# Performance work log

Hardware: AMD Instinct MI355X
Metric: run time of the kernel (lower is better)

The kernel has to match this reference:

```python
import jax, jax.numpy as jnp
import numpy as np

EPS = 1e-8

def setup_inputs() -> dict:
    key = jax.random.key(0)
    k1, k2, k3, k4, k5 = jax.random.split(key, 5)
    B, S, d, H = 4, 1024, 512, 8
    hd = d // H
    x = jax.random.normal(k1, (B, S, d), dtype=jnp.float32)
    V = jax.random.normal(k2, (B, S, H, hd), dtype=jnp.float32)
    # binary biological mask [B, S, S]
    M = (jax.random.uniform(k3, (B, S, S)) > 0.5).astype(jnp.float32)
    in_proj_w = jax.random.normal(k4, (3 * d, d), dtype=jnp.float32) * 0.02
    in_proj_b = jnp.zeros((3 * d,), dtype=jnp.float32)
    out_w = jax.random.normal(k5, (d, d), dtype=jnp.float32) * 0.02
    out_b = jnp.zeros((d,), dtype=jnp.float32)
    return {"x": x, "V": V, "M": M, "in_proj_w": in_proj_w,
            "in_proj_b": in_proj_b, "out_w": out_w, "out_b": out_b}


def reference(x, V, M, in_proj_w, in_proj_b, out_w, out_b):
    B, S, d = x.shape
    H, hd = V.shape[2], V.shape[3]
    # packed QKV projection (torch MHA in_proj); V slice is computed by torch
    # but its result is discarded, so only Q,K slices influence the output.
    qkv = x @ in_proj_w.T + in_proj_b            # [B, S, 3d]
    q = qkv[..., :d].reshape(B, S, H, hd).transpose(0, 2, 1, 3)        # [B,H,S,hd]
    k = qkv[..., d:2 * d].reshape(B, S, H, hd).transpose(0, 2, 1, 3)   # [B,H,S,hd]
    scores = jnp.einsum("bhqd,bhkd->bhqk", q, k) / jnp.sqrt(jnp.float32(hd))
    A = jax.nn.softmax(scores, axis=-1)           # [B,H,S,S] per-head attn weights
    # biological mask + L1 renormalization (post-hoc, as in original)
    A_sparse = A * M[:, None, :, :]
    norm = jnp.sum(jnp.abs(A_sparse), axis=-1, keepdims=True) + EPS
    A_bar = A_sparse / norm
    # custom V: [B,S,H,hd] -> [B,H,S,hd]
    Vp = V.transpose(0, 2, 1, 3)
    out = jnp.einsum("bhqk,bhkd->bhqd", A_bar, Vp)  # [B,H,S,hd]
    out = out.transpose(0, 2, 1, 3).reshape(B, S, d)
    return out @ out_w.T + out_b
```

## Files before the change

kernel.cpp:

```cpp
#include <hip/hip_runtime.h>
#include <hip/hip_bf16.h>

#define BB 4
#define SS 1024
#define DD 512
#define HH 8
#define HD 64

typedef __attribute__((ext_vector_type(8))) short bf16x8;
typedef __attribute__((ext_vector_type(4))) float f32x4;

static __device__ __forceinline__ unsigned short f2b(float f) {
  union { float f; unsigned int u; } c; c.f = f;
  return (unsigned short)((c.u + 0x7fffu + ((c.u >> 16) & 1u)) >> 16);
}

__global__ __launch_bounds__(256) void prep(
    const float* __restrict__ x, const float* __restrict__ W1,
    const float* __restrict__ Wo, const float* __restrict__ Mmask,
    const float* __restrict__ V, unsigned short* __restrict__ xb,
    unsigned short* __restrict__ W1b, unsigned short* __restrict__ Wob,
    unsigned char* __restrict__ Mpack, unsigned short* __restrict__ Vt) {
  __shared__ float Ls[64][65];
  const int bid = blockIdx.x;
  const int tid = threadIdx.x;

  if (bid < 1408) {
    const float* src; unsigned short* dst; size_t off;
    if (bid < 1024) { src = x;  dst = xb;  off = ((size_t)bid * 256 + tid) * 8; }
    else if (bid < 1280) { src = W1; dst = W1b; off = ((size_t)(bid - 1024) * 256 + tid) * 8; }
    else { src = Wo; dst = Wob; off = ((size_t)(bid - 1280) * 256 + tid) * 8; }
    const float4 a = *(const float4*)(src + off);
    const float4 b = *(const float4*)(src + off + 4);
    union { unsigned short s[8]; uint4 v; } o;
    o.s[0] = f2b(a.x); o.s[1] = f2b(a.y); o.s[2] = f2b(a.z); o.s[3] = f2b(a.w);
    o.s[4] = f2b(b.x); o.s[5] = f2b(b.y); o.s[6] = f2b(b.z); o.s[7] = f2b(b.w);
    *(uint4*)(dst + off) = o.v;
  } else if (bid < 3456) {
    const size_t g = (size_t)(bid - 1408) * 256 + tid;
    const float4 a = *(const float4*)(Mmask + g * 8);
    const float4 b = *(const float4*)(Mmask + g * 8 + 4);
    unsigned v = 0;
    v |= (a.x > 0.5f) ? 1u : 0u;   v |= (a.y > 0.5f) ? 2u : 0u;
    v |= (a.z > 0.5f) ? 4u : 0u;   v |= (a.w > 0.5f) ? 8u : 0u;
    v |= (b.x > 0.5f) ? 16u : 0u;  v |= (b.y > 0.5f) ? 32u : 0u;
    v |= (b.z > 0.5f) ? 64u : 0u;  v |= (b.w > 0.5f) ? 128u : 0u;
    Mpack[g] = (unsigned char)v;
  } else {
    const int id = bid - 3456;
    const int s0 = (id & 15) * 64, h = (id >> 4) & 7, b = id >> 7;
    {
      const int r = tid >> 2, cs = (tid & 3) * 16;
      const float* src = V + ((size_t)((b * SS + s0 + r) * HH) + h) * HD + cs;
#pragma unroll
      for (int j = 0; j < 4; j++) {
        const float4 v = *(const float4*)(src + j * 4);
        Ls[r][cs + j * 4 + 0] = v.x; Ls[r][cs + j * 4 + 1] = v.y;
        Ls[r][cs + j * 4 + 2] = v.z; Ls[r][cs + j * 4 + 3] = v.w;
      }
    }
    __syncthreads();
    {
      const int d = tid >> 2, ss = (tid & 3) * 16;
      union { unsigned short s[16]; uint4 v[2]; } o;
#pragma unroll
      for (int j = 0; j < 16; j++) o.s[j] = f2b(Ls[ss + j][d]);
      unsigned short* dst =
          Vt + ((size_t)((b * HH + h) * HD + d)) * SS + s0 + ss;
      *(uint4*)dst = o.v[0];
      *(uint4*)(dst + 8) = o.v[1];
    }
  }
}

__global__ __launch_bounds__(256) void gemm_qk(
    const unsigned short* __restrict__ xb, const unsigned short* __restrict__ W1b,
    const float* __restrict__ bias, unsigned short* __restrict__ qkb) {
  __shared__ unsigned short As[128][40];
  __shared__ unsigned short Bs[64][40];
  const int tid = threadIdx.x;
  const int lane = tid & 63, wave = tid >> 6;
  const int l16 = lane & 15, quad = lane >> 4;
  const int row0 = blockIdx.y * 128, col0 = blockIdx.x * 64;

  f32x4 acc[2][4];
#pragma unroll
  for (int i = 0; i < 2; i++)
#pragma unroll
    for (int j = 0; j < 4; j++) acc[i][j] = (f32x4){0.f, 0.f, 0.f, 0.f};

  const int ra = tid >> 1, csa = (tid & 1) * 16;
  const int rb = tid >> 2, csb = (tid & 3) * 8;
  const unsigned short* ap = xb + (size_t)(row0 + ra) * DD + csa;
  const unsigned short* bp = W1b + (size_t)(col0 + rb) * DD + csb;

  uint4 pa0 = *(const uint4*)ap, pa1 = *(const uint4*)(ap + 8);
  uint4 pb = *(const uint4*)bp;

  for (int k0 = 0; k0 < DD; k0 += 32) {
    __syncthreads();
    *(uint4*)&As[ra][csa] = pa0;
    *(uint4*)&As[ra][csa + 8] = pa1;
    *(uint4*)&Bs[rb][csb] = pb;
    __syncthreads();
    if (k0 + 32 < DD) {
      pa0 = *(const uint4*)(ap + k0 + 32);
      pa1 = *(const uint4*)(ap + k0 + 40);
      pb = *(const uint4*)(bp + k0 + 32);
    }

    const bf16x8 a0 = *(const bf16x8*)&As[wave * 32 + l16][quad * 8];
    const bf16x8 a1 = *(const bf16x8*)&As[wave * 32 + 16 + l16][quad * 8];
#pragma unroll
    for (int nt = 0; nt < 4; nt++) {
      const bf16x8 bb = *(const bf16x8*)&Bs[nt * 16 + l16][quad * 8];
      acc[0][nt] = __builtin_amdgcn_mfma_f32_16x16x32_bf16(a0, bb, acc[0][nt], 0, 0, 0);
      acc[1][nt] = __builtin_amdgcn_mfma_f32_16x16x32_bf16(a1, bb, acc[1][nt], 0, 0, 0);
    }
  }

#pragma unroll
  for (int nt = 0; nt < 4; nt++) {
    const int col = col0 + nt * 16 + l16;
    const float bv = bias[col];
    const float scale = (col < DD) ? 0.125f : 1.0f;
#pragma unroll
    for (int mi = 0; mi < 2; mi++)
#pragma unroll
      for (int reg = 0; reg < 4; reg++) {
        const int row = row0 + wave * 32 + mi * 16 + quad * 4 + reg;
        qkb[(size_t)row * 1024 + col] = f2b((acc[mi][nt][reg] + bv) * scale);
      }
  }
}

__global__ __launch_bounds__(256) void gemm_out(
    const unsigned short* __restrict__ Ab, const unsigned short* __restrict__ Wob,
    const float* __restrict__ bias, float* __restrict__ out) {
  __shared__ unsigned short As[64][40];
  __shared__ unsigned short Bs[64][40];
  const int tid = threadIdx.x;
  const int lane = tid & 63, wave = tid >> 6;
  const int l16 = lane & 15, quad = lane >> 4;
  const int row0 = blockIdx.y * 64, col0 = blockIdx.x * 64;

  f32x4 acc[4];
#pragma unroll
  for (int j = 0; j < 4; j++) acc[j] = (f32x4){0.f, 0.f, 0.f, 0.f};

  const int r = tid >> 2, cs = (tid & 3) * 8;
  const unsigned short* ap = Ab + (size_t)(row0 + r) * DD + cs;
  const unsigned short* bp = Wob + (size_t)(col0 + r) * DD + cs;

  uint4 pa = *(const uint4*)ap;
  uint4 pb = *(const uint4*)bp;

  for (int k0 = 0; k0 < DD; k0 += 32) {
    __syncthreads();
    *(uint4*)&As[r][cs] = pa;
    *(uint4*)&Bs[r][cs] = pb;
    __syncthreads();
    if (k0 + 32 < DD) {
      pa = *(const uint4*)(ap + k0 + 32);
      pb = *(const uint4*)(bp + k0 + 32);
    }

    const bf16x8 a0 = *(const bf16x8*)&As[wave * 16 + l16][quad * 8];
#pragma unroll
    for (int nt = 0; nt < 4; nt++) {
      const bf16x8 bb = *(const bf16x8*)&Bs[nt * 16 + l16][quad * 8];
      acc[nt] = __builtin_amdgcn_mfma_f32_16x16x32_bf16(a0, bb, acc[nt], 0, 0, 0);
    }
  }

#pragma unroll
  for (int nt = 0; nt < 4; nt++) {
    const int col = col0 + nt * 16 + l16;
    const float bv = bias[col];
#pragma unroll
    for (int reg = 0; reg < 4; reg++) {
      const int row = row0 + wave * 16 + quad * 4 + reg;
      out[(size_t)row * DD + col] = acc[nt][reg] + bv;
    }
  }
}

__global__ __launch_bounds__(256) void flash_attn_split(
    const unsigned short* __restrict__ qkb, const unsigned short* __restrict__ Vt,
    const unsigned char* __restrict__ Mpack, float* __restrict__ Opart,
    float* __restrict__ Sms) {
  __shared__ unsigned short QP[64][72];
  __shared__ unsigned short Ks[64][72];
  __shared__ unsigned short Vs[64][72];

  const int tid = threadIdx.x;
  const int lane = tid & 63, wave = tid >> 6;
  const int l16 = lane & 15, quad = lane >> 4;
  const int q0 = blockIdx.x * 64;
  const int h = blockIdx.y & 7, sp = blockIdx.y >> 3;
  const int b = blockIdx.z;

  const int r = tid >> 2, cs = (tid & 3) * 16;

  {
    const unsigned short* s = qkb + (size_t)(b * SS + q0 + r) * 1024 + h * HD + cs;
    *(uint4*)&QP[r][cs] = *(const uint4*)s;
    *(uint4*)&QP[r][cs + 8] = *(const uint4*)(s + 8);
  }

  union { uint4 v[4]; unsigned w[16]; } mu;
  {
    const uint4* mp = (const uint4*)(Mpack +
        (size_t)(b * SS + q0 + wave * 16 + l16) * 128 + sp * 64);
    mu.v[0] = mp[0]; mu.v[1] = mp[1]; mu.v[2] = mp[2]; mu.v[3] = mp[3];
  }

  __syncthreads();
  const bf16x8 bQ0 = *(const bf16x8*)&QP[wave * 16 + l16][quad * 8];
  const bf16x8 bQ1 = *(const bf16x8*)&QP[wave * 16 + l16][32 + quad * 8];
  unsigned short(*Ps)[72] = (unsigned short(*)[72]) & QP[wave * 16][0];

  float Smp = 0.f;
  f32x4 O[4];
#pragma unroll
  for (int i = 0; i < 4; i++) O[i] = (f32x4){0.f, 0.f, 0.f, 0.f};

  const unsigned short* kp =
      qkb + (size_t)(b * SS + sp * 8 * 64 + r) * 1024 + DD + h * HD + cs;
  const unsigned short* vp =
      Vt + ((size_t)((b * HH + h) * HD + r)) * SS + sp * 8 * 64 + cs;

  uint4 pk0 = *(const uint4*)kp, pk1 = *(const uint4*)(kp + 8);
  uint4 pv0 = *(const uint4*)vp, pv1 = *(const uint4*)(vp + 8);

#pragma unroll
  for (int i = 0; i < 8; i++) {
    const unsigned mlo = mu.w[2 * i], mhi = mu.w[2 * i + 1];

    __syncthreads();
    *(uint4*)&Ks[r][cs] = pk0;
    *(uint4*)&Ks[r][cs + 8] = pk1;
    *(uint4*)&Vs[r][cs] = pv0;
    *(uint4*)&Vs[r][cs + 8] = pv1;
    __syncthreads();

    if (i < 7) {
      const unsigned short* nk = kp + (size_t)(i + 1) * 64 * 1024;
      const unsigned short* nv = vp + (i + 1) * 64;
      pk0 = *(const uint4*)nk; pk1 = *(const uint4*)(nk + 8);
      pv0 = *(const uint4*)nv; pv1 = *(const uint4*)(nv + 8);
    }

#pragma unroll
    for (int t = 0; t < 4; t++) {
      const bf16x8 aK0 = *(const bf16x8*)&Ks[t * 16 + l16][quad * 8];
      const bf16x8 aK1 = *(const bf16x8*)&Ks[t * 16 + l16][32 + quad * 8];
      f32x4 a = (f32x4){0.f, 0.f, 0.f, 0.f};
      a = __builtin_amdgcn_mfma_f32_16x16x32_bf16(aK0, bQ0, a, 0, 0, 0);
      a = __builtin_amdgcn_mfma_f32_16x16x32_bf16(aK1, bQ1, a, 0, 0, 0);
      const unsigned nib =
          ((t < 2 ? mlo : mhi) >> ((t & 1) * 16 + quad * 4)) & 0xFu;
      float e0 = __expf(a[0]); e0 = (nib & 1u) ? e0 : 0.f;
      float e1 = __expf(a[1]); e1 = (nib & 2u) ? e1 : 0.f;
      float e2 = __expf(a[2]); e2 = (nib & 4u) ? e2 : 0.f;
      float e3 = __expf(a[3]); e3 = (nib & 8u) ? e3 : 0.f;
      Smp += (e0 + e1) + (e2 + e3);
      uint2 w;
      w.x = (unsigned)f2b(e0) | ((unsigned)f2b(e1) << 16);
      w.y = (unsigned)f2b(e2) | ((unsigned)f2b(e3) << 16);
      *(uint2*)&Ps[l16][t * 16 + quad * 4] = w;
    }

    const bf16x8 aP0 = *(const bf16x8*)&Ps[l16][quad * 8];
    const bf16x8 aP1 = *(const bf16x8*)&Ps[l16][32 + quad * 8];
#pragma unroll
    for (int dt = 0; dt < 4; dt++) {
      const bf16x8 bV0 = *(const bf16x8*)&Vs[dt * 16 + l16][quad * 8];
      const bf16x8 bV1 = *(const bf16x8*)&Vs[dt * 16 + l16][32 + quad * 8];
      O[dt] = __builtin_amdgcn_mfma_f32_16x16x32_bf16(aP0, bV0, O[dt], 0, 0, 0);
      O[dt] = __builtin_amdgcn_mfma_f32_16x16x32_bf16(aP1, bV1, O[dt], 0, 0, 0);
    }
  }

  Smp += __shfl_xor(Smp, 16);
  Smp += __shfl_xor(Smp, 32);
  const size_t grow0 = (size_t)(b * HH + h) * SS + q0 + wave * 16;
  const int NR = BB * HH * SS;
  if (lane < 16) Sms[(size_t)sp * NR + grow0 + lane] = Smp;
#pragma unroll
  for (int reg = 0; reg < 4; reg++) {
    const size_t obase = ((size_t)sp * NR + grow0 + quad * 4 + reg) * HD;
#pragma unroll
    for (int dt = 0; dt < 4; dt++)
      Opart[obase + dt * 16 + l16] = O[dt][reg];
  }
}

__global__ __launch_bounds__(256) void combine(
    const float* __restrict__ Opart, const float* __restrict__ Sms,
    unsigned short* __restrict__ attnb) {
  const int idx = blockIdx.x * 256 + threadIdx.x;
  const int row = idx >> 4;
  const int d = (idx & 15) * 4;
  const int NR = BB * HH * SS;
  const float4 o0 = *(const float4*)(Opart + (size_t)row * HD + d);
  const float4 o1 = *(const float4*)(Opart + ((size_t)NR + row) * HD + d);
  const float s = Sms[row] + Sms[NR + row];
  const float inv = 1.0f / (s + 1e-12f);
  const int b = row >> 13, h = (row >> 10) & 7, q = row & 1023;
  union { unsigned short us[4]; uint2 v; } o;
  o.us[0] = f2b((o0.x + o1.x) * inv);
  o.us[1] = f2b((o0.y + o1.y) * inv);
  o.us[2] = f2b((o0.z + o1.z) * inv);
  o.us[3] = f2b((o0.w + o1.w) * inv);
  *(uint2*)(attnb + (size_t)(b * SS + q) * DD + h * HD + d) = o.v;
}

extern "C" void kernel_launch(void* const* d_in, const int* in_sizes, int n_in,
                              void* d_out, int out_size, void* d_ws,
                              size_t ws_size, hipStream_t stream) {
  const float* x = (const float*)d_in[0];
  const float* V = (const float*)d_in[1];
  const float* Mmask = (const float*)d_in[2];
  const float* in_proj_w = (const float*)d_in[3];
  const float* in_proj_b = (const float*)d_in[4];
  const float* out_w = (const float*)d_in[5];
  const float* out_b = (const float*)d_in[6];
  float* out = (float*)d_out;

  unsigned char* ws = (unsigned char*)d_ws;
  unsigned short* qkb   = (unsigned short*)(ws);
  unsigned short* xb    = (unsigned short*)(ws + (8ull << 20));
  unsigned short* W1b   = (unsigned short*)(ws + (12ull << 20));
  unsigned short* Wob   = (unsigned short*)(ws + (13ull << 20));
  unsigned short* Vt    = (unsigned short*)(ws + (14ull << 20));
  unsigned short* attnb = (unsigned short*)(ws + (18ull << 20));
  float*          Opart = (float*)(ws + (22ull << 20));
  float*          Sms   = (float*)(ws + (38ull << 20));
  unsigned char*  Mpack = ws + (38ull << 20) + (256u << 10);

  prep<<<3968, 256, 0, stream>>>(x, in_proj_w, out_w, Mmask, V,
                                 xb, W1b, Wob, Mpack, Vt);
  gemm_qk<<<dim3(16, 32), 256, 0, stream>>>(xb, W1b, in_proj_b, qkb);
  flash_attn_split<<<dim3(SS / 64, 2 * HH, BB), 256, 0, stream>>>(
      qkb, Vt, Mpack, Opart, Sms);
  combine<<<2048, 256, 0, stream>>>(Opart, Sms, attnb);
  gemm_out<<<dim3(8, 64), 256, 0, stream>>>(attnb, Wob, out_b, out);
}
```

Baseline: 138.0 us.

## Fuse split-K attention halves and combine into one 512-thread block

The two key-range halves of attention, which used to run as separate blocks, now run as two wave groups inside a single 512-thread block. Their partial outputs and softmax sums are merged through shared memory, which removes the separate combine kernel and the fp32 partial-output round trip through global memory. The mask is now loaded per tile instead of all up front, which lowers register use. In exchange, more LDS is used per block and the grid has half as many blocks, which may reduce occupancy and parallelism.

```diff
diff --git a/kernel.cpp b/kernel.cpp
--- a/kernel.cpp
+++ b/kernel.cpp
@@ -185,81 +185,82 @@
   }
 }
 
-__global__ __launch_bounds__(256) void flash_attn_split(
+__global__ __launch_bounds__(512, 4) void flash_attn_fused(
     const unsigned short* __restrict__ qkb, const unsigned short* __restrict__ Vt,
-    const unsigned char* __restrict__ Mpack, float* __restrict__ Opart,
-    float* __restrict__ Sms) {
+    const unsigned char* __restrict__ Mpack, unsigned short* __restrict__ attnb) {
   __shared__ unsigned short QP[64][72];
-  __shared__ unsigned short Ks[64][72];
-  __shared__ unsigned short Vs[64][72];
+  __shared__ unsigned short P2[64][72];
+  __shared__ unsigned short Ks[2][64][72];
+  __shared__ unsigned short Vs[2][64][72];
+  __shared__ float SmS[2][64];
 
   const int tid = threadIdx.x;
   const int lane = tid & 63, wave = tid >> 6;
   const int l16 = lane & 15, quad = lane >> 4;
+  const int wq = wave & 3, sp = wave >> 2;
   const int q0 = blockIdx.x * 64;
-  const int h = blockIdx.y & 7, sp = blockIdx.y >> 3;
+  const int h = blockIdx.y;
   const int b = blockIdx.z;
 
-  const int r = tid >> 2, cs = (tid & 3) * 16;
+  const int r2 = tid >> 3, cs2 = (tid & 7) * 8;
 
   {
-    const unsigned short* s = qkb + (size_t)(b * SS + q0 + r) * 1024 + h * HD + cs;
-    *(uint4*)&QP[r][cs] = *(const uint4*)s;
-    *(uint4*)&QP[r][cs + 8] = *(const uint4*)(s + 8);
-  }
-
-  union { uint4 v[4]; unsigned w[16]; } mu;
-  {
-    const uint4* mp = (const uint4*)(Mpack +
-        (size_t)(b * SS + q0 + wave * 16 + l16) * 128 + sp * 64);
-    mu.v[0] = mp[0]; mu.v[1] = mp[1]; mu.v[2] = mp[2]; mu.v[3] = mp[3];
-  }
+    const unsigned short* s = qkb + (size_t)(b * SS + q0 + r2) * 1024 + h * HD + cs2;
+    *(uint4*)&QP[r2][cs2] = *(const uint4*)s;
+  }
+
+  const unsigned char* mp =
+      Mpack + (size_t)(b * SS + q0 + wq * 16 + l16) * 128 + sp * 64;
+  uint2 pm = *(const uint2*)mp;
 
   __syncthreads();
-  const bf16x8 bQ0 = *(const bf16x8*)&QP[wave * 16 + l16][quad * 8];
-  const bf16x8 bQ1 = *(const bf16x8*)&QP[wave * 16 + l16][32 + quad * 8];
-  unsigned short(*Ps)[72] = (unsigned short(*)[72]) & QP[wave * 16][0];
+  const bf16x8 bQ0 = *(const bf16x8*)&QP[wq * 16 + l16][quad * 8];
+  const bf16x8 bQ1 = *(const bf16x8*)&QP[wq * 16 + l16][32 + quad * 8];
+  unsigned short(*Ps)[72] =
+      (unsigned short(*)[72])(sp ? &P2[wq * 16][0] : &QP[wq * 16][0]);
 
   float Smp = 0.f;
   f32x4 O[4];
 #pragma unroll
   for (int i = 0; i < 4; i++) O[i] = (f32x4){0.f, 0.f, 0.f, 0.f};
 
-  const unsigned short* kp =
-      qkb + (size_t)(b * SS + sp * 8 * 64 + r) * 1024 + DD + h * HD + cs;
-  const unsigned short* vp =
-      Vt + ((size_t)((b * HH + h) * HD + r)) * SS + sp * 8 * 64 + cs;
-
-  uint4 pk0 = *(const uint4*)kp, pk1 = *(const uint4*)(kp + 8);
-  uint4 pv0 = *(const uint4*)vp, pv1 = *(const uint4*)(vp + 8);
+  const unsigned short* kp0 =
+      qkb + (size_t)(b * SS + r2) * 1024 + DD + h * HD + cs2;
+  const unsigned short* kp1 = kp0 + (size_t)512 * 1024;
+  const unsigned short* vp0 =
+      Vt + ((size_t)((b * HH + h) * HD + r2)) * SS + cs2;
+  const unsigned short* vp1 = vp0 + 512;
+
+  uint4 pk0 = *(const uint4*)kp0, pk1 = *(const uint4*)kp1;
+  uint4 pv0 = *(const uint4*)vp0, pv1 = *(const uint4*)vp1;
 
 #pragma unroll
   for (int i = 0; i < 8; i++) {
-    const unsigned mlo = mu.w[2 * i], mhi = mu.w[2 * i + 1];
-
-    __syncthreads();
-    *(uint4*)&Ks[r][cs] = pk0;
-    *(uint4*)&Ks[r][cs + 8] = pk1;
-    *(uint4*)&Vs[r][cs] = pv0;
-    *(uint4*)&Vs[r][cs + 8] = pv1;
-    __syncthreads();
-
+    __syncthreads();
+    *(uint4*)&Ks[0][r2][cs2] = pk0;
+    *(uint4*)&Ks[1][r2][cs2] = pk1;
+    *(uint4*)&Vs[0][r2][cs2] = pv0;
+    *(uint4*)&Vs[1][r2][cs2] = pv1;
+    __syncthreads();
+
+    const uint2 pm_cur = pm;
     if (i < 7) {
-      const unsigned short* nk = kp + (size_t)(i + 1) * 64 * 1024;
-      const unsigned short* nv = vp + (i + 1) * 64;
-      pk0 = *(const uint4*)nk; pk1 = *(const uint4*)(nk + 8);
-      pv0 = *(const uint4*)nv; pv1 = *(const uint4*)(nv + 8);
+      pk0 = *(const uint4*)(kp0 + (size_t)(i + 1) * 64 * 1024);
+      pk1 = *(const uint4*)(kp1 + (size_t)(i + 1) * 64 * 1024);
+      pv0 = *(const uint4*)(vp0 + (i + 1) * 64);
+      pv1 = *(const uint4*)(vp1 + (i + 1) * 64);
+      pm = *(const uint2*)(mp + (i + 1) * 8);
     }
 
 #pragma unroll
     for (int t = 0; t < 4; t++) {
-      const bf16x8 aK0 = *(const bf16x8*)&Ks[t * 16 + l16][quad * 8];
-      const bf16x8 aK1 = *(const bf16x8*)&Ks[t * 16 + l16][32 + quad * 8];
+      const bf16x8 aK0 = *(const bf16x8*)&Ks[sp][t * 16 + l16][quad * 8];
+      const bf16x8 aK1 = *(const bf16x8*)&Ks[sp][t * 16 + l16][32 + quad * 8];
       f32x4 a = (f32x4){0.f, 0.f, 0.f, 0.f};
       a = __builtin_amdgcn_mfma_f32_16x16x32_bf16(aK0, bQ0, a, 0, 0, 0);
       a = __builtin_amdgcn_mfma_f32_16x16x32_bf16(aK1, bQ1, a, 0, 0, 0);
       const unsigned nib =
-          ((t < 2 ? mlo : mhi) >> ((t & 1) * 16 + quad * 4)) & 0xFu;
+          ((t < 2 ? pm_cur.x : pm_cur.y) >> ((t & 1) * 16 + quad * 4)) & 0xFu;
       float e0 = __expf(a[0]); e0 = (nib & 1u) ? e0 : 0.f;
       float e1 = __expf(a[1]); e1 = (nib & 2u) ? e1 : 0.f;
       float e2 = __expf(a[2]); e2 = (nib & 4u) ? e2 : 0.f;
@@ -275,8 +276,8 @@
     const bf16x8 aP1 = *(const bf16x8*)&Ps[l16][32 + quad * 8];
 #pragma unroll
     for (int dt = 0; dt < 4; dt++) {
-      const bf16x8 bV0 = *(const bf16x8*)&Vs[dt * 16 + l16][quad * 8];
-      const bf16x8 bV1 = *(const bf16x8*)&Vs[dt * 16 + l16][32 + quad * 8];
+      const bf16x8 bV0 = *(const bf16x8*)&Vs[sp][dt * 16 + l16][quad * 8];
+      const bf16x8 bV1 = *(const bf16x8*)&Vs[sp][dt * 16 + l16][32 + quad * 8];
       O[dt] = __builtin_amdgcn_mfma_f32_16x16x32_bf16(aP0, bV0, O[dt], 0, 0, 0);
       O[dt] = __builtin_amdgcn_mfma_f32_16x16x32_bf16(aP1, bV1, O[dt], 0, 0, 0);
     }
@@ -284,36 +285,35 @@
 
   Smp += __shfl_xor(Smp, 16);
   Smp += __shfl_xor(Smp, 32);
-  const size_t grow0 = (size_t)(b * HH + h) * SS + q0 + wave * 16;
-  const int NR = BB * HH * SS;
-  if (lane < 16) Sms[(size_t)sp * NR + grow0 + lane] = Smp;
-#pragma unroll
-  for (int reg = 0; reg < 4; reg++) {
-    const size_t obase = ((size_t)sp * NR + grow0 + quad * 4 + reg) * HD;
+  if (lane < 16) SmS[sp][wq * 16 + lane] = Smp;
+
+  __syncthreads();
+  float* Of = reinterpret_cast<float*>(&Ks[0][0][0]);
+  if (sp == 1) {
 #pragma unroll
     for (int dt = 0; dt < 4; dt++)
-      Opart[obase + dt * 16 + l16] = O[dt][reg];
-  }
-}
-
-__global__ __launch_bounds__(256) void combine(
-    const float* __restrict__ Opart, const float* __restrict__ Sms,
-    unsigned short* __restrict__ attnb) {
-  const int idx = blockIdx.x * 256 + threadIdx.x;
-  const int row = idx >> 4;
-  const int d = (idx & 15) * 4;
-  const int NR = BB * HH * SS;
-  const float4 o0 = *(const float4*)(Opart + (size_t)row * HD + d);
-  const float4 o1 = *(const float4*)(Opart + ((size_t)NR + row) * HD + d);
-  const float s = Sms[row] + Sms[NR + row];
-  const float inv = 1.0f / (s + 1e-12f);
-  const int b = row >> 13, h = (row >> 10) & 7, q = row & 1023;
-  union { unsigned short us[4]; uint2 v; } o;
-  o.us[0] = f2b((o0.x + o1.x) * inv);
-  o.us[1] = f2b((o0.y + o1.y) * inv);
-  o.us[2] = f2b((o0.z + o1.z) * inv);
-  o.us[3] = f2b((o0.w + o1.w) * inv);
-  *(uint2*)(attnb + (size_t)(b * SS + q) * DD + h * HD + d) = o.v;
+#pragma unroll
+      for (int reg = 0; reg < 4; reg++)
+        Of[(wq * 16 + quad * 4 + reg) * 64 + dt * 16 + l16] = O[dt][reg];
+  }
+  __syncthreads();
+
+  if (sp == 0) {
+    float inv[4];
+#pragma unroll
+    for (int reg = 0; reg < 4; reg++) {
+      const int ql = wq * 16 + quad * 4 + reg;
+      inv[reg] = 1.0f / (SmS[0][ql] + SmS[1][ql] + 1e-12f);
+    }
+#pragma unroll
+    for (int dt = 0; dt < 4; dt++)
+#pragma unroll
+      for (int reg = 0; reg < 4; reg++) {
+        const int ql = wq * 16 + quad * 4 + reg;
+        const float v = (O[dt][reg] + Of[ql * 64 + dt * 16 + l16]) * inv[reg];
+        attnb[(size_t)(b * SS + q0 + ql) * DD + h * HD + dt * 16 + l16] = f2b(v);
+      }
+  }
 }
 
 extern "C" void kernel_launch(void* const* d_in, const int* in_sizes, int n_in,
@@ -335,15 +335,12 @@
   unsigned short* Wob   = (unsigned short*)(ws + (13ull << 20));
   unsigned short* Vt    = (unsigned short*)(ws + (14ull << 20));
   unsigned short* attnb = (unsigned short*)(ws + (18ull << 20));
-  float*          Opart = (float*)(ws + (22ull << 20));
-  float*          Sms   = (float*)(ws + (38ull << 20));
   unsigned char*  Mpack = ws + (38ull << 20) + (256u << 10);
 
   prep<<<3968, 256, 0, stream>>>(x, in_proj_w, out_w, Mmask, V,
                                  xb, W1b, Wob, Mpack, Vt);
   gemm_qk<<<dim3(16, 32), 256, 0, stream>>>(xb, W1b, in_proj_b, qkb);
-  flash_attn_split<<<dim3(SS / 64, 2 * HH, BB), 256, 0, stream>>>(
-      qkb, Vt, Mpack, Opart, Sms);
-  combine<<<2048, 256, 0, stream>>>(Opart, Sms, attnb);
+  flash_attn_fused<<<dim3(SS / 64, HH, BB), 512, 0, stream>>>(
+      qkb, Vt, Mpack, attnb);
   gemm_out<<<dim3(8, 64), 256, 0, stream>>>(attnb, Wob, out_b, out);
 }
```

Result: no change. 135.5 us (-1.8%).
